# Kernel tuning notes

Measured on AMD Instinct MI355X. Metric: run time of the kernel, lower is better.

Reference implementation:

```python
import jax, jax.numpy as jnp
import numpy as np

B, S, E, D, V, H, NL = 16, 1024, 64, 256, 10000, 8, 3
HD = D // H


def _ln(x, g, b):
    m = jnp.mean(x, -1, keepdims=True)
    v = jnp.mean((x - m) ** 2, -1, keepdims=True)
    return (x - m) / jnp.sqrt(v + 1e-5) * g + b


def _mha(q_in, kv_in, in_w, in_b, out_w, out_b, causal):
    # torch nn.MultiheadAttention with packed in_proj [3D, D]
    d = q_in.shape[-1]
    q = q_in @ in_w[:d].T + in_b[:d]
    k = kv_in @ in_w[d:2 * d].T + in_b[d:2 * d]
    v = kv_in @ in_w[2 * d:].T + in_b[2 * d:]
    sp = lambda t: t.reshape(t.shape[0], t.shape[1], H, HD).transpose(0, 2, 1, 3)
    q, k, v = sp(q), sp(k), sp(v)
    s = jnp.einsum('bhqd,bhkd->bhqk', q, k) / jnp.float32(np.sqrt(HD))
    if causal:
        L = s.shape[-1]
        s = jnp.where(jnp.tril(jnp.ones((L, L), bool)), s, jnp.float32(-1e30))
    a = jax.nn.softmax(s, -1)
    o = jnp.einsum('bhqk,bhkd->bhqd', a, v).transpose(0, 2, 1, 3).reshape(q_in.shape[0], -1, d)
    return o @ out_w.T + out_b


def setup_inputs() -> dict:
    key = jax.random.key(0)
    ks = iter(jax.random.split(key, 40))
    n = lambda *sh: jax.random.normal(next(ks), sh, jnp.float32) * 0.05
    d = dict(
        tractovka=n(B, E), context=n(B, E), card=n(B, E),
        enc_w=n(3, D, E), enc_b=n(3, D),
        enc_ln_g=jnp.ones((3, D), jnp.float32), enc_ln_b=jnp.zeros((3, D), jnp.float32),
        fusion_w=n(D, 3 * D), fusion_b=n(D),
        fusion_ln_g=jnp.ones(D, jnp.float32), fusion_ln_b=jnp.zeros(D, jnp.float32),
        tok_emb=n(V, D), pos_emb=n(1024, D),
        sa_in_w=n(NL, 3 * D, D), sa_in_b=n(NL, 3 * D), sa_out_w=n(NL, D, D), sa_out_b=n(NL, D),
        ca_in_w=n(NL, 3 * D, D), ca_in_b=n(NL, 3 * D), ca_out_w=n(NL, D, D), ca_out_b=n(NL, D),
        ln1_g=jnp.ones((NL, D), jnp.float32), ln1_b=jnp.zeros((NL, D), jnp.float32),
        ln2_g=jnp.ones((NL, D), jnp.float32), ln2_b=jnp.zeros((NL, D), jnp.float32),
        ln3_g=jnp.ones((NL, D), jnp.float32), ln3_b=jnp.zeros((NL, D), jnp.float32),
        ffn_w1=n(NL, 4 * D, D), ffn_b1=n(NL, 4 * D), ffn_w2=n(NL, D, 4 * D), ffn_b2=n(NL, D),
        out_w=n(V, D), out_b=n(V),
        prev_tokens=jax.random.randint(next(ks), (B, S), 0, V, jnp.int32),
    )
    return d


def reference(tractovka, context, card, enc_w, enc_b, enc_ln_g, enc_ln_b,
              fusion_w, fusion_b, fusion_ln_g, fusion_ln_b, tok_emb, pos_emb,
              sa_in_w, sa_in_b, sa_out_w, sa_out_b, ca_in_w, ca_in_b, ca_out_w, ca_out_b,
              ln1_g, ln1_b, ln2_g, ln2_b, ln3_g, ln3_b,
              ffn_w1, ffn_b1, ffn_w2, ffn_b2, out_w, out_b, prev_tokens):
    enc = lambda x, i: jax.nn.gelu(_ln(x @ enc_w[i].T + enc_b[i], enc_ln_g[i], enc_ln_b[i]), approximate=False)
    mem = jnp.concatenate([enc(tractovka, 0), enc(context, 1), enc(card, 2)], -1)
    mem = jax.nn.gelu(_ln(mem @ fusion_w.T + fusion_b, fusion_ln_g, fusion_ln_b), approximate=False)[:, None, :]  # [B,1,D]
    x = tok_emb[prev_tokens] + pos_emb[:prev_tokens.shape[1]][None]  # [B,S,D]
    for i in range(NL):  # post-norm decoder layer: self-attn, cross-attn, ReLU FFN
        x = _ln(x + _mha(x, x, sa_in_w[i], sa_in_b[i], sa_out_w[i], sa_out_b[i], True), ln1_g[i], ln1_b[i])
        x = _ln(x + _mha(x, mem, ca_in_w[i], ca_in_b[i], ca_out_w[i], ca_out_b[i], False), ln2_g[i], ln2_b[i])
        x = _ln(x + (jax.nn.relu(x @ ffn_w1[i].T + ffn_b1[i]) @ ffn_w2[i].T + ffn_b2[i]), ln3_g[i], ln3_b[i])
    return x @ out_w.T + out_b  # [B,S,V]
```

## Files before the change

kernel.cpp:

```cpp
#include <hip/hip_runtime.h>
#include <math.h>

constexpr int B = 16, S = 1024, D = 256, E = 64, H = 8, HD = 32;

typedef __attribute__((ext_vector_type(8))) short bf16x8;
typedef __attribute__((ext_vector_type(4))) short bf16x4;
typedef __attribute__((ext_vector_type(4))) float f32x4;

__device__ __forceinline__ float gelu_f(float x) {
  return 0.5f * x * (1.0f + erff(x * 0.70710678118654752440f));
}

__device__ __forceinline__ unsigned short f2bf(float f) {
  union { float f; unsigned u; } x; x.f = f;
  unsigned r = x.u + 0x7fff + ((x.u >> 16) & 1);
  return (unsigned short)(r >> 16);
}

__device__ __forceinline__ unsigned cvt_pk_bf16(float a, float b) {
  unsigned r;
  asm("v_cvt_pk_bf16_f32 %0, %1, %2" : "=v"(r) : "v"(a), "v"(b));
  return r;
}

__device__ __forceinline__ void gl16(const void* g, void* l) {
  __builtin_amdgcn_global_load_lds(
      (const __attribute__((address_space(1))) void*)g,
      (__attribute__((address_space(3))) void*)l, 16, 0, 0);
}

__global__ void k_cvt(const float* __restrict__ src, unsigned short* __restrict__ dst, int n) {
  int i = (blockIdx.x * 256 + threadIdx.x) * 4;
  if (i >= n) return;
  float4 v = *(const float4*)(src + i);
  dst[i + 0] = f2bf(v.x);
  dst[i + 1] = f2bf(v.y);
  dst[i + 2] = f2bf(v.z);
  dst[i + 3] = f2bf(v.w);
}

__global__ void k_embed(const int* __restrict__ tok,
                        const float* __restrict__ tok_emb,
                        const float* __restrict__ pos_emb,
                        float* __restrict__ x, unsigned short* __restrict__ xb) {
  int bs = blockIdx.x;
  int d = threadIdx.x;
  int s = bs & (S - 1);
  int t = tok[bs];
  float v = tok_emb[(size_t)t * D + d] + pos_emb[s * D + d];
  x[(size_t)bs * D + d] = v;
  xb[(size_t)bs * D + d] = f2bf(v);
}

__global__ void k_enc(const float* __restrict__ tr, const float* __restrict__ ctx,
                      const float* __restrict__ card,
                      const float* __restrict__ w, const float* __restrict__ bias,
                      const float* __restrict__ g, const float* __restrict__ bt,
                      float* __restrict__ cat) {
  int b = blockIdx.x, i = blockIdx.y, d = threadIdx.x;
  const float* xin = (i == 0 ? tr : (i == 1 ? ctx : card)) + b * E;
  const float* wr = w + ((size_t)i * D + d) * E;
  float acc = bias[i * D + d];
#pragma unroll 8
  for (int e = 0; e < E; ++e) acc += xin[e] * wr[e];
  __shared__ float s1[D], s2[D];
  s1[d] = acc; s2[d] = acc * acc;
  __syncthreads();
  for (int o = D / 2; o > 0; o >>= 1) {
    if (d < o) { s1[d] += s1[d + o]; s2[d] += s2[d + o]; }
    __syncthreads();
  }
  float mean = s1[0] * (1.0f / D);
  float var = s2[0] * (1.0f / D) - mean * mean;
  float nv = (acc - mean) * rsqrtf(var + 1e-5f) * g[i * D + d] + bt[i * D + d];
  cat[(size_t)b * (3 * D) + i * D + d] = gelu_f(nv);
}

__global__ void k_fusion(const float* __restrict__ cat, const float* __restrict__ w,
                         const float* __restrict__ bias, const float* __restrict__ g,
                         const float* __restrict__ bt, float* __restrict__ mem) {
  int b = blockIdx.x, d = threadIdx.x;
  const float* xr = cat + (size_t)b * (3 * D);
  const float* wr = w + (size_t)d * (3 * D);
  float acc = bias[d];
  for (int k = 0; k < 3 * D; ++k) acc += xr[k] * wr[k];
  __shared__ float s1[D], s2[D];
  s1[d] = acc; s2[d] = acc * acc;
  __syncthreads();
  for (int o = D / 2; o > 0; o >>= 1) {
    if (d < o) { s1[d] += s1[d + o]; s2[d] += s2[d + o]; }
    __syncthreads();
  }
  float mean = s1[0] * (1.0f / D);
  float var = s2[0] * (1.0f / D) - mean * mean;
  float nv = (acc - mean) * rsqrtf(var + 1e-5f) * g[d] + bt[d];
  mem[(size_t)b * D + d] = gelu_f(nv);
}

__global__ void k_ca(const float* __restrict__ mem,
                     const float* __restrict__ in_w, const float* __restrict__ in_b,
                     const float* __restrict__ out_w, const float* __restrict__ out_b,
                     float* __restrict__ ca_add) {
  int b = blockIdx.x, l = blockIdx.y, d = threadIdx.x;
  const float* mr = mem + (size_t)b * D;
  const float* wi = in_w + ((size_t)l * 3 * D + 2 * D + d) * D;
  float v = in_b[(size_t)l * 3 * D + 2 * D + d];
  for (int k = 0; k < D; ++k) v += mr[k] * wi[k];
  __shared__ float vs[D];
  vs[d] = v;
  __syncthreads();
  const float* wo = out_w + ((size_t)l * D + d) * D;
  float o = out_b[(size_t)l * D + d];
  for (int k = 0; k < D; ++k) o += vs[k] * wo[k];
  ca_add[((size_t)l * B + b) * D + d] = o;
}

__global__ __launch_bounds__(512)
void k_attn6(const unsigned short* __restrict__ qkv, unsigned short* __restrict__ out) {
  constexpr int KT = 64;
  __shared__ unsigned short Ks[2][KT * 32];
  __shared__ unsigned short Vt[2][32 * KT];
  __shared__ unsigned short Pl[8 * 32 * KT];

  const int t = threadIdx.x;
  const int w = t >> 6, lane = t & 63;
  const int lg = lane >> 4, lr = lane & 15;
  const int bh = blockIdx.y;
  const int h = bh & (H - 1), b = bh >> 3;
  const int qtile = (int)gridDim.x - 1 - (int)blockIdx.x;
  const int qb = qtile << 8;
  const int qw = qb + w * 32;
  const unsigned short* base = qkv + (size_t)b * S * 768 + h * HD;

  bf16x8 qf[2];
#pragma unroll
  for (int qr = 0; qr < 2; ++qr)
    qf[qr] = *(const bf16x8*)(base + (size_t)(qw + qr * 16 + lr) * 768 + lg * 8);

  f32x4 o[2][2];
#pragma unroll
  for (int qr = 0; qr < 2; ++qr)
#pragma unroll
    for (int dt = 0; dt < 2; ++dt) o[qr][dt] = (f32x4){0.f, 0.f, 0.f, 0.f};
  float mq[2], lq[2];
#pragma unroll
  for (int qr = 0; qr < 2; ++qr) { mq[qr] = -3.0e38f; lq[qr] = 0.f; }

  const float Cs = 0.17677669529663687f * 1.4426950408889634f;

  const int skey = t >> 2;
  const int sch = (t & 3) * 8;
  const int vkey = t >> 3;
  const int vch = (t & 7) * 4;
  char* pbase = (char*)Pl + (w << 12);

  const int nkt = (qb + 256) >> 6;

  if (t < 256) gl16(base + (size_t)skey * 768 + 256 + sch, (char*)Ks[0] + t * 16);
  bf16x4 vv = *(const bf16x4*)(base + (size_t)vkey * 768 + 512 + vch);
  __syncthreads();

  for (int kti = 0; kti < nkt; ++kti) {
    const int kt = kti << 6;
    const int cur = kti & 1;

#pragma unroll
    for (int j = 0; j < 4; ++j) {
      int d = vch + j;
      int byteo = d * (KT * 2) + ((vkey * 2) ^ ((d & 7) << 4));
      *(unsigned short*)((char*)Vt[cur] + byteo) = (unsigned short)vv[j];
    }
    if (kti + 1 < nkt) {
      if (t < 256)
        gl16(base + (size_t)(kt + KT + skey) * 768 + 256 + sch, (char*)Ks[cur ^ 1] + t * 16);
      vv = *(const bf16x4*)(base + (size_t)(kt + KT + vkey) * 768 + 512 + vch);
    }

    const bool active = (kt <= qw + 31);
    if (active) {
      bf16x8 kf[4];
#pragma unroll
      for (int t4 = 0; t4 < 4; ++t4)
        kf[t4] = *(const bf16x8*)&Ks[cur][(t4 * 16 + lr) * 32 + lg * 8];
      f32x4 sc[2][4];
      __builtin_amdgcn_s_setprio(1);
#pragma unroll
      for (int qr = 0; qr < 2; ++qr)
#pragma unroll
        for (int t4 = 0; t4 < 4; ++t4)
          sc[qr][t4] = __builtin_amdgcn_mfma_f32_16x16x32_bf16(
              kf[t4], qf[qr], (f32x4){0.f, 0.f, 0.f, 0.f}, 0, 0, 0);
      __builtin_amdgcn_s_setprio(0);

      if (kt + KT > qw) {
#pragma unroll
        for (int qr = 0; qr < 2; ++qr) {
          int q = qw + qr * 16 + lr;
#pragma unroll
          for (int t4 = 0; t4 < 4; ++t4)
#pragma unroll
            for (int r = 0; r < 4; ++r) {
              int k = kt + t4 * 16 + lg * 4 + r;
              if (k > q) sc[qr][t4][r] = -3.0e38f;
            }
        }
      }

#pragma unroll
      for (int qr = 0; qr < 2; ++qr) {
        float mx = sc[qr][0][0];
#pragma unroll
        for (int t4 = 0; t4 < 4; ++t4)
#pragma unroll
          for (int r = 0; r < 4; ++r) mx = fmaxf(mx, sc[qr][t4][r]);
        mx = fmaxf(mx, __shfl_xor(mx, 16));
        mx = fmaxf(mx, __shfl_xor(mx, 32));
        if (__any(mx > mq[qr] + 8.0f)) {
          float mn = fmaxf(mx, mq[qr]);
          float cf = exp2f((mq[qr] - mn) * Cs);
          mq[qr] = mn;
          lq[qr] *= cf;
#pragma unroll
          for (int r = 0; r < 4; ++r) {
            float cfo = __shfl(cf, (lane & 48) | (lg * 4 + r));
            o[qr][0][r] *= cfo;
            o[qr][1][r] *= cfo;
          }
        }
        float nmxC = -mq[qr] * Cs;
        float ps = 0.f;
#pragma unroll
        for (int t4 = 0; t4 < 4; ++t4)
#pragma unroll
          for (int r = 0; r < 4; ++r) {
            float p = exp2f(fmaf(sc[qr][t4][r], Cs, nmxC));
            sc[qr][t4][r] = p;
            ps += p;
          }
        lq[qr] += ps;
        int ql = qr * 16 + lr;
        int swz = (ql & 7) << 4;
        char* prow = pbase + ql * (KT * 2);
#pragma unroll
        for (int t4 = 0; t4 < 4; ++t4) {
          unsigned lo = cvt_pk_bf16(sc[qr][t4][0], sc[qr][t4][1]);
          unsigned hi = cvt_pk_bf16(sc[qr][t4][2], sc[qr][t4][3]);
          *(uint2*)(prow + ((t4 * 32 + lg * 8) ^ swz)) = make_uint2(lo, hi);
        }
      }
    }

    __syncthreads();

    if (active) {
#pragma unroll
      for (int kp = 0; kp < 2; ++kp) {
        bf16x8 vf[2], pf[2];
        int kb = kp * 64 + lg * 16;
#pragma unroll
        for (int dt = 0; dt < 2; ++dt) {
          int d = dt * 16 + lr;
          vf[dt] = *(const bf16x8*)((char*)Vt[cur] + d * (KT * 2) + (kb ^ ((d & 7) << 4)));
        }
#pragma unroll
        for (int qr = 0; qr < 2; ++qr) {
          int ql = qr * 16 + lr;
          pf[qr] = *(const bf16x8*)(pbase + ql * (KT * 2) + (kb ^ ((ql & 7) << 4)));
        }
        __builtin_amdgcn_s_setprio(1);
#pragma unroll
        for (int qr = 0; qr < 2; ++qr)
#pragma unroll
          for (int dt = 0; dt < 2; ++dt)
            o[qr][dt] = __builtin_amdgcn_mfma_f32_16x16x32_bf16(
                pf[qr], vf[dt], o[qr][dt], 0, 0, 0);
        __builtin_amdgcn_s_setprio(0);
      }
    }
  }

#pragma unroll
  for (int qr = 0; qr < 2; ++qr) {
    float ls = lq[qr];
    ls += __shfl_xor(ls, 16);
    ls += __shfl_xor(ls, 32);
    float invq = 1.0f / ls;
#pragma unroll
    for (int r = 0; r < 4; ++r) {
      float inv = __shfl(invq, (lane & 48) | (lg * 4 + r));
      int q = qw + qr * 16 + lg * 4 + r;
      unsigned short* orow = out + (size_t)(b * S + q) * D + h * HD;
#pragma unroll
      for (int dt = 0; dt < 2; ++dt)
        orow[dt * 16 + lr] = f2bf(o[qr][dt][r] * inv);
    }
  }
}

template <int EPI, int OUTBF>
__global__ __launch_bounds__(256)
void k_gemm_mfma(const unsigned short* __restrict__ A,
                 const unsigned short* __restrict__ W,
                 const float* __restrict__ bias,
                 void* __restrict__ Cout,
                 int M, int N, int K) {
  __shared__ unsigned short As[128][32];
  __shared__ unsigned short Bs[128][32];
  int t = threadIdx.x;
  int row0 = blockIdx.y * 128, col0 = blockIdx.x * 128;
  int wid = t >> 6, lane = t & 63;
  int wr = wid >> 1, wc = wid & 1;
  int lrow = lane & 15, lko = (lane >> 4) * 8;

  f32x4 acc[4][4];
#pragma unroll
  for (int mi = 0; mi < 4; ++mi)
#pragma unroll
    for (int ni = 0; ni < 4; ++ni)
      acc[mi][ni] = (f32x4){0.f, 0.f, 0.f, 0.f};

  int c0 = t, c1 = t + 256;
  int ar0 = c0 >> 2, aq0 = (c0 & 3) * 8;
  int ar1 = c1 >> 2, aq1 = (c1 & 3) * 8;
  int wrow0 = col0 + ar0; if (wrow0 > N - 1) wrow0 = N - 1;
  int wrow1 = col0 + ar1; if (wrow1 > N - 1) wrow1 = N - 1;

  const unsigned short* A0 = A + (size_t)(row0 + ar0) * K + aq0;
  const unsigned short* A1 = A + (size_t)(row0 + ar1) * K + aq1;
  const unsigned short* W0 = W + (size_t)wrow0 * K + aq0;
  const unsigned short* W1 = W + (size_t)wrow1 * K + aq1;

  for (int kt = 0; kt < K; kt += 32) {
    gl16(A0 + kt, (char*)As + c0 * 16);
    gl16(A1 + kt, (char*)As + c1 * 16);
    gl16(W0 + kt, (char*)Bs + c0 * 16);
    gl16(W1 + kt, (char*)Bs + c1 * 16);
    __syncthreads();

    bf16x8 af[4], bfr[4];
#pragma unroll
    for (int mi = 0; mi < 4; ++mi)
      af[mi] = *(const bf16x8*)&As[wr * 64 + mi * 16 + lrow][lko];
#pragma unroll
    for (int ni = 0; ni < 4; ++ni)
      bfr[ni] = *(const bf16x8*)&Bs[wc * 64 + ni * 16 + lrow][lko];
#pragma unroll
    for (int mi = 0; mi < 4; ++mi)
#pragma unroll
      for (int ni = 0; ni < 4; ++ni)
        acc[mi][ni] = __builtin_amdgcn_mfma_f32_16x16x32_bf16(af[mi], bfr[ni], acc[mi][ni], 0, 0, 0);
    __syncthreads();
  }

  int rbase = row0 + wr * 64 + (lane >> 4) * 4;
  int cbase = col0 + wc * 64 + lrow;
#pragma unroll
  for (int ni = 0; ni < 4; ++ni) {
    int c = cbase + ni * 16;
    if (c < N) {
      float bv = bias[c];
#pragma unroll
      for (int mi = 0; mi < 4; ++mi) {
        int rr = rbase + mi * 16;
#pragma unroll
        for (int r = 0; r < 4; ++r) {
          float v = acc[mi][ni][r] + bv;
          if (EPI == 1) v = fmaxf(v, 0.0f);
          size_t off = (size_t)(rr + r) * N + c;
          if (OUTBF)
            ((unsigned short*)Cout)[off] = f2bf(v);
          else
            ((float*)Cout)[off] = v;
        }
      }
    }
  }
}

template <int NLN>
__global__ __launch_bounds__(256)
void k_gemm_ln(const unsigned short* __restrict__ A,
               const unsigned short* __restrict__ W,
               const float* __restrict__ bias,
               const float* __restrict__ res,
               const float* __restrict__ ca,
               const float* __restrict__ g1, const float* __restrict__ b1,
               const float* __restrict__ g2, const float* __restrict__ b2,
               float* __restrict__ xout, unsigned short* __restrict__ xb,
               int K) {
  __shared__ unsigned short As[2][64][32];
  __shared__ unsigned short Bs[2][256][32];
  __shared__ float red[2][64][4];
  int t = threadIdx.x;
  int row0 = blockIdx.x * 64;
  int wc = t >> 6, lane = t & 63;
  int lr = lane & 15, lg = lane >> 4;

  f32x4 acc[4][4];
#pragma unroll
  for (int mi = 0; mi < 4; ++mi)
#pragma unroll
    for (int ni = 0; ni < 4; ++ni)
      acc[mi][ni] = (f32x4){0.f, 0.f, 0.f, 0.f};

  const unsigned short* srcs[5];
  char* dsts[2][5];
#pragma unroll
  for (int i = 0; i < 5; ++i) {
    int c = t + (i << 8);
    if (c < 256) {
      int rw = c >> 2, q = (c & 3) * 8;
      srcs[i] = A + (size_t)(row0 + rw) * K + q;
      dsts[0][i] = (char*)As[0] + c * 16;
      dsts[1][i] = (char*)As[1] + c * 16;
    } else {
      int cb = c - 256;
      int rw = cb >> 2, q = (cb & 3) * 8;
      srcs[i] = W + (size_t)rw * K + q;
      dsts[0][i] = (char*)Bs[0] + cb * 16;
      dsts[1][i] = (char*)Bs[1] + cb * 16;
    }
  }

  const int nsteps = K >> 5;
#pragma unroll
  for (int i = 0; i < 5; ++i) gl16(srcs[i], dsts[0][i]);
  __syncthreads();

  for (int s = 0; s < nsteps; ++s) {
    const int cur = s & 1;
    if (s + 1 < nsteps) {
      int off = (s + 1) << 5;
#pragma unroll
      for (int i = 0; i < 5; ++i) gl16(srcs[i] + off, dsts[cur ^ 1][i]);
    }
    bf16x8 af[4], bfr[4];
#pragma unroll
    for (int mi = 0; mi < 4; ++mi)
      af[mi] = *(const bf16x8*)&As[cur][mi * 16 + lr][lg * 8];
#pragma unroll
    for (int ni = 0; ni < 4; ++ni)
      bfr[ni] = *(const bf16x8*)&Bs[cur][wc * 64 + ni * 16 + lr][lg * 8];
    __builtin_amdgcn_s_setprio(1);
#pragma unroll
    for (int mi = 0; mi < 4; ++mi)
#pragma unroll
      for (int ni = 0; ni < 4; ++ni)
        acc[mi][ni] = __builtin_amdgcn_mfma_f32_16x16x32_bf16(af[mi], bfr[ni], acc[mi][ni], 0, 0, 0);
    __builtin_amdgcn_s_setprio(0);
    __syncthreads();
  }

  int colb = wc * 64 + lr;
  float mean[4][4], rstd[4][4];

#pragma unroll
  for (int mi = 0; mi < 4; ++mi) {
#pragma unroll
    for (int r = 0; r < 4; ++r) {
      int rowl = mi * 16 + lg * 4 + r;
      int rowg = row0 + rowl;
      float s1 = 0.f, s2 = 0.f;
#pragma unroll
      for (int ni = 0; ni < 4; ++ni) {
        int c = colb + ni * 16;
        float v = acc[mi][ni][r] + bias[c] + res[(size_t)rowg * D + c];
        acc[mi][ni][r] = v;
        s1 += v; s2 += v * v;
      }
#pragma unroll
      for (int msk = 1; msk <= 8; msk <<= 1) {
        s1 += __shfl_xor(s1, msk);
        s2 += __shfl_xor(s2, msk);
      }
      if (lr == 0) { red[0][rowl][wc] = s1; red[1][rowl][wc] = s2; }
    }
  }
  __syncthreads();
#pragma unroll
  for (int mi = 0; mi < 4; ++mi)
#pragma unroll
    for (int r = 0; r < 4; ++r) {
      int rowl = mi * 16 + lg * 4 + r;
      f32x4 a = *(const f32x4*)&red[0][rowl][0];
      f32x4 bq = *(const f32x4*)&red[1][rowl][0];
      float s1 = a[0] + a[1] + a[2] + a[3];
      float s2 = bq[0] + bq[1] + bq[2] + bq[3];
      float mn = s1 * (1.0f / D);
      float vr = s2 * (1.0f / D) - mn * mn;
      mean[mi][r] = mn;
      rstd[mi][r] = rsqrtf(vr + 1e-5f);
    }
#pragma unroll
  for (int mi = 0; mi < 4; ++mi)
#pragma unroll
    for (int ni = 0; ni < 4; ++ni) {
      int c = colb + ni * 16;
      float gg = g1[c], bb = b1[c];
#pragma unroll
      for (int r = 0; r < 4; ++r)
        acc[mi][ni][r] = (acc[mi][ni][r] - mean[mi][r]) * rstd[mi][r] * gg + bb;
    }

  if (NLN == 2) {
    __syncthreads();
#pragma unroll
    for (int mi = 0; mi < 4; ++mi) {
#pragma unroll
      for (int r = 0; r < 4; ++r) {
        int rowl = mi * 16 + lg * 4 + r;
        int rowg = row0 + rowl;
        int bidx = rowg >> 10;
        float s1 = 0.f, s2 = 0.f;
#pragma unroll
        for (int ni = 0; ni < 4; ++ni) {
          int c = colb + ni * 16;
          float v = acc[mi][ni][r] + ca[(size_t)bidx * D + c];
          acc[mi][ni][r] = v;
          s1 += v; s2 += v * v;
        }
#pragma unroll
        for (int msk = 1; msk <= 8; msk <<= 1) {
          s1 += __shfl_xor(s1, msk);
          s2 += __shfl_xor(s2, msk);
        }
        if (lr == 0) { red[0][rowl][wc] = s1; red[1][rowl][wc] = s2; }
      }
    }
    __syncthreads();
#pragma unroll
    for (int mi = 0; mi < 4; ++mi)
#pragma unroll
      for (int r = 0; r < 4; ++r) {
        int rowl = mi * 16 + lg * 4 + r;
        f32x4 a = *(const f32x4*)&red[0][rowl][0];
        f32x4 bq = *(const f32x4*)&red[1][rowl][0];
        float s1 = a[0] + a[1] + a[2] + a[3];
        float s2 = bq[0] + bq[1] + bq[2] + bq[3];
        float mn = s1 * (1.0f / D);
        float vr = s2 * (1.0f / D) - mn * mn;
        mean[mi][r] = mn;
        rstd[mi][r] = rsqrtf(vr + 1e-5f);
      }
#pragma unroll
    for (int mi = 0; mi < 4; ++mi)
#pragma unroll
      for (int ni = 0; ni < 4; ++ni) {
        int c = colb + ni * 16;
        float gg = g2[c], bb = b2[c];
#pragma unroll
        for (int r = 0; r < 4; ++r)
          acc[mi][ni][r] = (acc[mi][ni][r] - mean[mi][r]) * rstd[mi][r] * gg + bb;
      }
  }

#pragma unroll
  for (int mi = 0; mi < 4; ++mi)
#pragma unroll
    for (int r = 0; r < 4; ++r) {
      int rowg = row0 + mi * 16 + lg * 4 + r;
#pragma unroll
      for (int ni = 0; ni < 4; ++ni) {
        int c = colb + ni * 16;
        float v = acc[mi][ni][r];
        xout[(size_t)rowg * D + c] = v;
        xb[(size_t)rowg * D + c] = f2bf(v);
      }
    }
}

extern "C" void kernel_launch(void* const* d_in, const int* in_sizes, int n_in,
                              void* d_out, int out_size, void* d_ws, size_t ws_size,
                              hipStream_t stream) {
  (void)in_sizes; (void)n_in; (void)out_size; (void)ws_size;
  const float* tractovka = (const float*)d_in[0];
  const float* context   = (const float*)d_in[1];
  const float* card      = (const float*)d_in[2];
  const float* enc_w     = (const float*)d_in[3];
  const float* enc_b     = (const float*)d_in[4];
  const float* enc_ln_g  = (const float*)d_in[5];
  const float* enc_ln_b  = (const float*)d_in[6];
  const float* fusion_w  = (const float*)d_in[7];
  const float* fusion_b  = (const float*)d_in[8];
  const float* fusion_ln_g = (const float*)d_in[9];
  const float* fusion_ln_b = (const float*)d_in[10];
  const float* tok_emb   = (const float*)d_in[11];
  const float* pos_emb   = (const float*)d_in[12];
  const float* sa_in_w   = (const float*)d_in[13];
  const float* sa_in_b   = (const float*)d_in[14];
  const float* sa_out_w  = (const float*)d_in[15];
  const float* sa_out_b  = (const float*)d_in[16];
  const float* ca_in_w   = (const float*)d_in[17];
  const float* ca_in_b   = (const float*)d_in[18];
  const float* ca_out_w  = (const float*)d_in[19];
  const float* ca_out_b  = (const float*)d_in[20];
  const float* ln1_g     = (const float*)d_in[21];
  const float* ln1_b     = (const float*)d_in[22];
  const float* ln2_g     = (const float*)d_in[23];
  const float* ln2_b     = (const float*)d_in[24];
  const float* ln3_g     = (const float*)d_in[25];
  const float* ln3_b     = (const float*)d_in[26];
  const float* ffn_w1    = (const float*)d_in[27];
  const float* ffn_b1    = (const float*)d_in[28];
  const float* ffn_w2    = (const float*)d_in[29];
  const float* ffn_b2    = (const float*)d_in[30];
  const float* out_w     = (const float*)d_in[31];
  const float* out_b     = (const float*)d_in[32];
  const int*   prev      = (const int*)d_in[33];
  float* out = (float*)d_out;

  const int M = B * S;

  float* ws = (float*)d_ws;
  float* x      = ws;
  float* bufA   = x + (size_t)M * D;
  float* bufB   = bufA + (size_t)M * 768;
  float* cat    = bufB + (size_t)M * D;
  float* mem    = cat + (size_t)B * 3 * D;
  float* ca_add = mem + (size_t)B * D;
  unsigned short* xb    = (unsigned short*)(ca_add + (size_t)3 * B * D);
  unsigned short* attnb = xb + (size_t)M * D;
  unsigned short* wbf   = attnb + (size_t)M * D;
  unsigned short* qkvb  = (unsigned short*)bufA;
  unsigned short* ffn1b = (unsigned short*)bufA;

  const int n_qkvw = 3 * 768 * D;
  const int n_outw = 3 * D * D;
  const int n_f1w  = 3 * 1024 * D;
  const int n_f2w  = 3 * D * 1024;
  const int n_vw   = 10000 * D;
  unsigned short* w_qkv = wbf;
  unsigned short* w_out = w_qkv + n_qkvw;
  unsigned short* w_f1  = w_out + n_outw;
  unsigned short* w_f2  = w_f1 + n_f1w;
  unsigned short* w_v   = w_f2 + n_f2w;

  k_cvt<<<(n_qkvw / 4 + 255) / 256, 256, 0, stream>>>(sa_in_w, w_qkv, n_qkvw);
  k_cvt<<<(n_outw / 4 + 255) / 256, 256, 0, stream>>>(sa_out_w, w_out, n_outw);
  k_cvt<<<(n_f1w / 4 + 255) / 256, 256, 0, stream>>>(ffn_w1, w_f1, n_f1w);
  k_cvt<<<(n_f2w / 4 + 255) / 256, 256, 0, stream>>>(ffn_w2, w_f2, n_f2w);
  k_cvt<<<(n_vw / 4 + 255) / 256, 256, 0, stream>>>(out_w, w_v, n_vw);

  k_embed<<<M, D, 0, stream>>>(prev, tok_emb, pos_emb, x, xb);
  k_enc<<<dim3(B, 3), D, 0, stream>>>(tractovka, context, card, enc_w, enc_b,
                                      enc_ln_g, enc_ln_b, cat);
  k_fusion<<<B, D, 0, stream>>>(cat, fusion_w, fusion_b, fusion_ln_g, fusion_ln_b, mem);
  k_ca<<<dim3(B, 3), D, 0, stream>>>(mem, ca_in_w, ca_in_b, ca_out_w, ca_out_b, ca_add);

  for (int l = 0; l < 3; ++l) {
    k_gemm_mfma<0, 1><<<dim3(6, M / 128), 256, 0, stream>>>(
        xb, w_qkv + (size_t)l * 768 * D, sa_in_b + (size_t)l * 3 * D, qkvb,
        M, 768, D);
    k_attn6<<<dim3(S / 256, B * H), 512, 0, stream>>>(qkvb, attnb);
    k_gemm_ln<2><<<dim3(M / 64), 256, 0, stream>>>(
        attnb, w_out + (size_t)l * D * D, sa_out_b + (size_t)l * D,
        x, ca_add + (size_t)l * B * D,
        ln1_g + (size_t)l * D, ln1_b + (size_t)l * D,
        ln2_g + (size_t)l * D, ln2_b + (size_t)l * D,
        x, xb, D);
    k_gemm_mfma<1, 1><<<dim3(8, M / 128), 256, 0, stream>>>(
        xb, w_f1 + (size_t)l * 1024 * D, ffn_b1 + (size_t)l * 4 * D, ffn1b,
        M, 1024, D);
    k_gemm_ln<1><<<dim3(M / 64), 256, 0, stream>>>(
        ffn1b, w_f2 + (size_t)l * D * 1024, ffn_b2 + (size_t)l * D,
        x, nullptr,
        ln3_g + (size_t)l * D, ln3_b + (size_t)l * D,
        nullptr, nullptr,
        x, xb, 1024);
  }
  k_gemm_mfma<0, 0><<<dim3(79, M / 128), 256, 0, stream>>>(
      xb, w_v, out_b, out, M, 10000, D);
}
```

Measured before the change: 816.3 us.

## Merge setup kernels, deepen gemm_ln pipeline, swizzle vocab GEMM block order

Folds the five weight-conversion launches into one k_cvt_all kernel and merges the encoder, fusion and cross-attention side path into a single k_side kernel that reduces with wave shuffles. The embedding kernel is vectorized to float4 loads with packed bf16 stores. k_gemm_ln moves from double to four-slot LDS buffering with two stages in flight, using explicit vmcnt waits and one barrier per step. The final vocab projection GEMM remaps block indices so consecutive blocks spread across the grid, aiming at better cache reuse. The main risks are the hand-tuned vmcnt counts, where a wrong count corrupts results, and the extra LDS use in gemm_ln, which may lower occupancy.

New measurement: 825.6 us. Within noise of the previous version (+1.1%).

```diff
diff --git a/kernel.cpp b/kernel.cpp
--- a/kernel.cpp
+++ b/kernel.cpp
@@ -29,10 +29,18 @@
       (__attribute__((address_space(3))) void*)l, 16, 0, 0);
 }
 
-__global__ void k_cvt(const float* __restrict__ src, unsigned short* __restrict__ dst, int n) {
+__global__ void k_cvt_all(const float* __restrict__ s0, const float* __restrict__ s1,
+                          const float* __restrict__ s2, const float* __restrict__ s3,
+                          const float* __restrict__ s4, unsigned short* __restrict__ dst) {
   int i = (blockIdx.x * 256 + threadIdx.x) * 4;
-  if (i >= n) return;
-  float4 v = *(const float4*)(src + i);
+  const float* src;
+  int off;
+  if (i < 589824)       { src = s0; off = i; }
+  else if (i < 786432)  { src = s1; off = i - 589824; }
+  else if (i < 1572864) { src = s2; off = i - 786432; }
+  else if (i < 2359296) { src = s3; off = i - 1572864; }
+  else                  { src = s4; off = i - 2359296; }
+  float4 v = *(const float4*)(src + off);
   dst[i + 0] = f2bf(v.x);
   dst[i + 1] = f2bf(v.y);
   dst[i + 2] = f2bf(v.z);
@@ -43,76 +51,86 @@
                         const float* __restrict__ tok_emb,
                         const float* __restrict__ pos_emb,
                         float* __restrict__ x, unsigned short* __restrict__ xb) {
-  int bs = blockIdx.x;
-  int d = threadIdx.x;
-  int s = bs & (S - 1);
-  int t = tok[bs];
-  float v = tok_emb[(size_t)t * D + d] + pos_emb[s * D + d];
-  x[(size_t)bs * D + d] = v;
-  xb[(size_t)bs * D + d] = f2bf(v);
-}
-
-__global__ void k_enc(const float* __restrict__ tr, const float* __restrict__ ctx,
-                      const float* __restrict__ card,
-                      const float* __restrict__ w, const float* __restrict__ bias,
-                      const float* __restrict__ g, const float* __restrict__ bt,
-                      float* __restrict__ cat) {
-  int b = blockIdx.x, i = blockIdx.y, d = threadIdx.x;
-  const float* xin = (i == 0 ? tr : (i == 1 ? ctx : card)) + b * E;
-  const float* wr = w + ((size_t)i * D + d) * E;
-  float acc = bias[i * D + d];
+  int t = threadIdx.x;
+  int r = blockIdx.x * 4 + (t >> 6);
+  int c4 = (t & 63) * 4;
+  int s = r & (S - 1);
+  int tk = tok[r];
+  float4 te = *(const float4*)(tok_emb + (size_t)tk * D + c4);
+  float4 pe = *(const float4*)(pos_emb + (size_t)s * D + c4);
+  float4 v = make_float4(te.x + pe.x, te.y + pe.y, te.z + pe.z, te.w + pe.w);
+  *(float4*)(x + (size_t)r * D + c4) = v;
+  unsigned lo = cvt_pk_bf16(v.x, v.y), hi = cvt_pk_bf16(v.z, v.w);
+  *(uint2*)(xb + (size_t)r * D + c4) = make_uint2(lo, hi);
+}
+
+__global__ __launch_bounds__(256)
+void k_side(const float* __restrict__ tr, const float* __restrict__ ctx,
+            const float* __restrict__ card,
+            const float* __restrict__ enc_w, const float* __restrict__ enc_b,
+            const float* __restrict__ eg, const float* __restrict__ ebt,
+            const float* __restrict__ fw, const float* __restrict__ fb,
+            const float* __restrict__ fg, const float* __restrict__ fbt,
+            const float* __restrict__ ca_in_w, const float* __restrict__ ca_in_b,
+            const float* __restrict__ ca_out_w, const float* __restrict__ ca_out_b,
+            float* __restrict__ ca_add) {
+  int b = blockIdx.x, d = threadIdx.x;
+  __shared__ float catl[768], meml[256], vs[256];
+  __shared__ float rw1[4], rw2[4];
+
+  auto lnstat = [&](float acc, float& mean, float& rstd) {
+    float a1 = acc, a2 = acc * acc;
+#pragma unroll
+    for (int off = 32; off > 0; off >>= 1) {
+      a1 += __shfl_xor(a1, off);
+      a2 += __shfl_xor(a2, off);
+    }
+    int wid = d >> 6, lane = d & 63;
+    if (lane == 0) { rw1[wid] = a1; rw2[wid] = a2; }
+    __syncthreads();
+    float s1 = rw1[0] + rw1[1] + rw1[2] + rw1[3];
+    float s2 = rw2[0] + rw2[1] + rw2[2] + rw2[3];
+    mean = s1 * (1.0f / D);
+    float var = s2 * (1.0f / D) - mean * mean;
+    rstd = rsqrtf(var + 1e-5f);
+    __syncthreads();
+  };
+
+  for (int i = 0; i < 3; ++i) {
+    const float* xin = (i == 0 ? tr : (i == 1 ? ctx : card)) + b * E;
+    const float* wr = enc_w + ((size_t)i * D + d) * E;
+    float acc = enc_b[i * D + d];
 #pragma unroll 8
-  for (int e = 0; e < E; ++e) acc += xin[e] * wr[e];
-  __shared__ float s1[D], s2[D];
-  s1[d] = acc; s2[d] = acc * acc;
+    for (int e = 0; e < E; ++e) acc += xin[e] * wr[e];
+    float mean, rstd;
+    lnstat(acc, mean, rstd);
+    float nv = (acc - mean) * rstd * eg[i * D + d] + ebt[i * D + d];
+    catl[i * D + d] = gelu_f(nv);
+  }
   __syncthreads();
-  for (int o = D / 2; o > 0; o >>= 1) {
-    if (d < o) { s1[d] += s1[d + o]; s2[d] += s2[d + o]; }
-    __syncthreads();
-  }
-  float mean = s1[0] * (1.0f / D);
-  float var = s2[0] * (1.0f / D) - mean * mean;
-  float nv = (acc - mean) * rsqrtf(var + 1e-5f) * g[i * D + d] + bt[i * D + d];
-  cat[(size_t)b * (3 * D) + i * D + d] = gelu_f(nv);
-}
-
-__global__ void k_fusion(const float* __restrict__ cat, const float* __restrict__ w,
-                         const float* __restrict__ bias, const float* __restrict__ g,
-                         const float* __restrict__ bt, float* __restrict__ mem) {
-  int b = blockIdx.x, d = threadIdx.x;
-  const float* xr = cat + (size_t)b * (3 * D);
-  const float* wr = w + (size_t)d * (3 * D);
-  float acc = bias[d];
-  for (int k = 0; k < 3 * D; ++k) acc += xr[k] * wr[k];
-  __shared__ float s1[D], s2[D];
-  s1[d] = acc; s2[d] = acc * acc;
+
+  {
+    const float* fwr = fw + (size_t)d * 768;
+    float fa = fb[d];
+    for (int k = 0; k < 768; ++k) fa += catl[k] * fwr[k];
+    float mean, rstd;
+    lnstat(fa, mean, rstd);
+    meml[d] = gelu_f((fa - mean) * rstd * fg[d] + fbt[d]);
+  }
   __syncthreads();
-  for (int o = D / 2; o > 0; o >>= 1) {
-    if (d < o) { s1[d] += s1[d + o]; s2[d] += s2[d + o]; }
-    __syncthreads();
-  }
-  float mean = s1[0] * (1.0f / D);
-  float var = s2[0] * (1.0f / D) - mean * mean;
-  float nv = (acc - mean) * rsqrtf(var + 1e-5f) * g[d] + bt[d];
-  mem[(size_t)b * D + d] = gelu_f(nv);
-}
-
-__global__ void k_ca(const float* __restrict__ mem,
-                     const float* __restrict__ in_w, const float* __restrict__ in_b,
-                     const float* __restrict__ out_w, const float* __restrict__ out_b,
-                     float* __restrict__ ca_add) {
-  int b = blockIdx.x, l = blockIdx.y, d = threadIdx.x;
-  const float* mr = mem + (size_t)b * D;
-  const float* wi = in_w + ((size_t)l * 3 * D + 2 * D + d) * D;
-  float v = in_b[(size_t)l * 3 * D + 2 * D + d];
-  for (int k = 0; k < D; ++k) v += mr[k] * wi[k];
-  __shared__ float vs[D];
-  vs[d] = v;
-  __syncthreads();
-  const float* wo = out_w + ((size_t)l * D + d) * D;
-  float o = out_b[(size_t)l * D + d];
-  for (int k = 0; k < D; ++k) o += vs[k] * wo[k];
-  ca_add[((size_t)l * B + b) * D + d] = o;
+
+  for (int l = 0; l < 3; ++l) {
+    const float* wi = ca_in_w + ((size_t)l * 768 + 512 + d) * 256;
+    float v = ca_in_b[l * 768 + 512 + d];
+    for (int k = 0; k < 256; ++k) v += meml[k] * wi[k];
+    vs[d] = v;
+    __syncthreads();
+    const float* wo = ca_out_w + ((size_t)l * 256 + d) * 256;
+    float o = ca_out_b[l * 256 + d];
+    for (int k = 0; k < 256; ++k) o += vs[k] * wo[k];
+    ca_add[((size_t)l * B + b) * 256 + d] = o;
+    __syncthreads();
+  }
 }
 
 __global__ __launch_bounds__(512)
@@ -297,7 +315,7 @@
   }
 }
 
-template <int EPI, int OUTBF>
+template <int EPI, int OUTBF, int SWZ>
 __global__ __launch_bounds__(256)
 void k_gemm_mfma(const unsigned short* __restrict__ A,
                  const unsigned short* __restrict__ W,
@@ -307,7 +325,16 @@
   __shared__ unsigned short As[128][32];
   __shared__ unsigned short Bs[128][32];
   int t = threadIdx.x;
-  int row0 = blockIdx.y * 128, col0 = blockIdx.x * 128;
+  int bx = blockIdx.x, by = blockIdx.y;
+  if (SWZ) {
+    int nx = gridDim.x;
+    int lin = by * nx + bx;
+    int q = (nx * (int)gridDim.y) >> 3;
+    int nl = (lin & 7) * q + (lin >> 3);
+    by = nl / nx;
+    bx = nl - by * nx;
+  }
+  int row0 = by * 128, col0 = bx * 128;
   int wid = t >> 6, lane = t & 63;
   int wr = wid >> 1, wc = wid & 1;
   int lrow = lane & 15, lko = (lane >> 4) * 8;
@@ -388,8 +415,8 @@
                const float* __restrict__ g2, const float* __restrict__ b2,
                float* __restrict__ xout, unsigned short* __restrict__ xb,
                int K) {
-  __shared__ unsigned short As[2][64][32];
-  __shared__ unsigned short Bs[2][256][32];
+  __shared__ unsigned short As[4][64][32];
+  __shared__ unsigned short Bs[4][256][32];
   __shared__ float red[2][64][4];
   int t = threadIdx.x;
   int row0 = blockIdx.x * 64;
@@ -403,44 +430,49 @@
     for (int ni = 0; ni < 4; ++ni)
       acc[mi][ni] = (f32x4){0.f, 0.f, 0.f, 0.f};
 
-  const unsigned short* srcs[5];
-  char* dsts[2][5];
-#pragma unroll
-  for (int i = 0; i < 5; ++i) {
-    int c = t + (i << 8);
-    if (c < 256) {
-      int rw = c >> 2, q = (c & 3) * 8;
-      srcs[i] = A + (size_t)(row0 + rw) * K + q;
-      dsts[0][i] = (char*)As[0] + c * 16;
-      dsts[1][i] = (char*)As[1] + c * 16;
+  int arw = t >> 2, aq = (t & 3) * 8;
+  const unsigned short* srcA = A + (size_t)(row0 + arw) * K + aq;
+  int adoff = t * 16;
+  const unsigned short* srcB[4];
+  int bdoff[4];
+#pragma unroll
+  for (int j = 0; j < 4; ++j) {
+    int cb = t + (j << 8);
+    int rw = cb >> 2, q = (cb & 3) * 8;
+    srcB[j] = W + (size_t)rw * K + q;
+    bdoff[j] = cb * 16;
+  }
+
+  auto stage = [&](int s) {
+    int slot = s & 3;
+    int off = s << 5;
+    gl16(srcA + off, (char*)As[slot] + adoff);
+#pragma unroll
+    for (int j = 0; j < 4; ++j) gl16(srcB[j] + off, (char*)Bs[slot] + bdoff[j]);
+  };
+
+  const int nsteps = K >> 5;
+  stage(0);
+  stage(1);
+  for (int s = 0; s < nsteps; ++s) {
+    if (s + 2 < nsteps) {
+      stage(s + 2);
+      asm volatile("s_waitcnt vmcnt(10)" ::: "memory");
+    } else if (s + 1 < nsteps) {
+      asm volatile("s_waitcnt vmcnt(5)" ::: "memory");
     } else {
-      int cb = c - 256;
-      int rw = cb >> 2, q = (cb & 3) * 8;
-      srcs[i] = W + (size_t)rw * K + q;
-      dsts[0][i] = (char*)Bs[0] + cb * 16;
-      dsts[1][i] = (char*)Bs[1] + cb * 16;
-    }
-  }
-
-  const int nsteps = K >> 5;
-#pragma unroll
-  for (int i = 0; i < 5; ++i) gl16(srcs[i], dsts[0][i]);
-  __syncthreads();
-
-  for (int s = 0; s < nsteps; ++s) {
-    const int cur = s & 1;
-    if (s + 1 < nsteps) {
-      int off = (s + 1) << 5;
-#pragma unroll
-      for (int i = 0; i < 5; ++i) gl16(srcs[i] + off, dsts[cur ^ 1][i]);
-    }
+      asm volatile("s_waitcnt vmcnt(0)" ::: "memory");
+    }
+    __builtin_amdgcn_s_barrier();
+    __builtin_amdgcn_sched_barrier(0);
+    int slot = s & 3;
     bf16x8 af[4], bfr[4];
 #pragma unroll
     for (int mi = 0; mi < 4; ++mi)
-      af[mi] = *(const bf16x8*)&As[cur][mi * 16 + lr][lg * 8];
+      af[mi] = *(const bf16x8*)&As[slot][mi * 16 + lr][lg * 8];
 #pragma unroll
     for (int ni = 0; ni < 4; ++ni)
-      bfr[ni] = *(const bf16x8*)&Bs[cur][wc * 64 + ni * 16 + lr][lg * 8];
+      bfr[ni] = *(const bf16x8*)&Bs[slot][wc * 64 + ni * 16 + lr][lg * 8];
     __builtin_amdgcn_s_setprio(1);
 #pragma unroll
     for (int mi = 0; mi < 4; ++mi)
@@ -448,7 +480,6 @@
       for (int ni = 0; ni < 4; ++ni)
         acc[mi][ni] = __builtin_amdgcn_mfma_f32_16x16x32_bf16(af[mi], bfr[ni], acc[mi][ni], 0, 0, 0);
     __builtin_amdgcn_s_setprio(0);
-    __syncthreads();
   }
 
   int colb = wc * 64 + lr;
@@ -628,27 +659,22 @@
   const int n_outw = 3 * D * D;
   const int n_f1w  = 3 * 1024 * D;
   const int n_f2w  = 3 * D * 1024;
-  const int n_vw   = 10000 * D;
   unsigned short* w_qkv = wbf;
   unsigned short* w_out = w_qkv + n_qkvw;
   unsigned short* w_f1  = w_out + n_outw;
   unsigned short* w_f2  = w_f1 + n_f1w;
   unsigned short* w_v   = w_f2 + n_f2w;
 
-  k_cvt<<<(n_qkvw / 4 + 255) / 256, 256, 0, stream>>>(sa_in_w, w_qkv, n_qkvw);
-  k_cvt<<<(n_outw / 4 + 255) / 256, 256, 0, stream>>>(sa_out_w, w_out, n_outw);
-  k_cvt<<<(n_f1w / 4 + 255) / 256, 256, 0, stream>>>(ffn_w1, w_f1, n_f1w);
-  k_cvt<<<(n_f2w / 4 + 255) / 256, 256, 0, stream>>>(ffn_w2, w_f2, n_f2w);
-  k_cvt<<<(n_vw / 4 + 255) / 256, 256, 0, stream>>>(out_w, w_v, n_vw);
-
-  k_embed<<<M, D, 0, stream>>>(prev, tok_emb, pos_emb, x, xb);
-  k_enc<<<dim3(B, 3), D, 0, stream>>>(tractovka, context, card, enc_w, enc_b,
-                                      enc_ln_g, enc_ln_b, cat);
-  k_fusion<<<B, D, 0, stream>>>(cat, fusion_w, fusion_b, fusion_ln_g, fusion_ln_b, mem);
-  k_ca<<<dim3(B, 3), D, 0, stream>>>(mem, ca_in_w, ca_in_b, ca_out_w, ca_out_b, ca_add);
+  k_cvt_all<<<4804, 256, 0, stream>>>(sa_in_w, sa_out_w, ffn_w1, ffn_w2, out_w, wbf);
+
+  k_embed<<<M / 4, 256, 0, stream>>>(prev, tok_emb, pos_emb, x, xb);
+  k_side<<<B, 256, 0, stream>>>(tractovka, context, card,
+                                enc_w, enc_b, enc_ln_g, enc_ln_b,
+                                fusion_w, fusion_b, fusion_ln_g, fusion_ln_b,
+                                ca_in_w, ca_in_b, ca_out_w, ca_out_b, ca_add);
 
   for (int l = 0; l < 3; ++l) {
-    k_gemm_mfma<0, 1><<<dim3(6, M / 128), 256, 0, stream>>>(
+    k_gemm_mfma<0, 1, 0><<<dim3(6, M / 128), 256, 0, stream>>>(
         xb, w_qkv + (size_t)l * 768 * D, sa_in_b + (size_t)l * 3 * D, qkvb,
         M, 768, D);
     k_attn6<<<dim3(S / 256, B * H), 512, 0, stream>>>(qkvb, attnb);
@@ -658,7 +684,7 @@
         ln1_g + (size_t)l * D, ln1_b + (size_t)l * D,
         ln2_g + (size_t)l * D, ln2_b + (size_t)l * D,
         x, xb, D);
-    k_gemm_mfma<1, 1><<<dim3(8, M / 128), 256, 0, stream>>>(
+    k_gemm_mfma<1, 1, 0><<<dim3(8, M / 128), 256, 0, stream>>>(
         xb, w_f1 + (size_t)l * 1024 * D, ffn_b1 + (size_t)l * 4 * D, ffn1b,
         M, 1024, D);
     k_gemm_ln<1><<<dim3(M / 64), 256, 0, stream>>>(
@@ -668,6 +694,6 @@
         nullptr, nullptr,
         x, xb, 1024);
   }
-  k_gemm_mfma<0, 0><<<dim3(79, M / 128), 256, 0, stream>>>(
+  k_gemm_mfma<0, 0, 1><<<dim3(79, M / 128), 256, 0, stream>>>(
       xb, w_v, out_b, out, M, 10000, D);
 }
```
